# Kernel optimization log

Hardware: AMD Instinct MI355X
Metric: run time of the kernel (lower is better)

Reference implementation:

```python
import jax, jax.numpy as jnp
import numpy as np

N = 100000
E = 1600000
IN_C = 128
HID = 8
HEADS = 8
OUT_C = 40
NEG_SLOPE = 0.2


def _segment_softmax(e, seg, n):
    # e: [E, H], softmax over edges sharing the same destination `seg`
    m = jax.ops.segment_max(e, seg, num_segments=n)
    a = jnp.exp(e - m[seg])
    s = jax.ops.segment_sum(a, seg, num_segments=n)
    return a / (s[seg] + 1e-16)


def _gat_layer(x, src, dst, W, a_src, a_dst, b, heads, concat):
    # PyG GATConv (single-tensor input, shared lin for src/dst), self-loops pre-added.
    n = x.shape[0]
    c = W.shape[0] // heads
    h = (x @ W.T).reshape(n, heads, c)                     # [N, H, C]
    al_s = jnp.einsum('nhc,hc->nh', h, a_src)              # [N, H]
    al_d = jnp.einsum('nhc,hc->nh', h, a_dst)
    e = jax.nn.leaky_relu(al_s[src] + al_d[dst], NEG_SLOPE)  # [E, H]
    alpha = _segment_softmax(e, dst, n)                    # [E, H]
    out = jax.ops.segment_sum(alpha[:, :, None] * h[src], dst, num_segments=n)
    if concat:
        return out.reshape(n, heads * c) + b
    return out.mean(axis=1) + b


def setup_inputs() -> dict:
    key = jax.random.key(0)
    ks = jax.random.split(key, 24)
    HC = HEADS * HID
    def g(k, shape, fan_in):
        return jax.random.normal(k, shape, dtype=jnp.float32) * (1.0 / np.sqrt(fan_in))
    inp = {
        'x': jax.random.normal(ks[0], (N, IN_C), dtype=jnp.float32),
        'edge_index': jax.random.randint(ks[1], (2, E), 0, N, dtype=jnp.int32),
        # layer 0: in -> hidden x heads (concat)
        'W0': g(ks[2], (HC, IN_C), IN_C),
        'as0': g(ks[3], (HEADS, HID), HID),
        'ad0': g(ks[4], (HEADS, HID), HID),
        'b0': jnp.zeros((HC,), jnp.float32),
        'sW0': g(ks[5], (HC, IN_C), IN_C),
        'sb0': jnp.zeros((HC,), jnp.float32),
        # layer 1: HC -> hidden x heads (concat)
        'W1': g(ks[6], (HC, HC), HC),
        'as1': g(ks[7], (HEADS, HID), HID),
        'ad1': g(ks[8], (HEADS, HID), HID),
        'b1': jnp.zeros((HC,), jnp.float32),
        'sW1': g(ks[9], (HC, HC), HC),
        'sb1': jnp.zeros((HC,), jnp.float32),
        # layer 2: HC -> out (concat=False, mean over heads)
        'W2': g(ks[10], (HEADS * OUT_C, HC), HC),
        'as2': g(ks[11], (HEADS, OUT_C), OUT_C),
        'ad2': g(ks[12], (HEADS, OUT_C), OUT_C),
        'b2': jnp.zeros((OUT_C,), jnp.float32),
        'sW2': g(ks[13], (OUT_C, HC), HC),
        'sb2': jnp.zeros((OUT_C,), jnp.float32),
    }
    return inp


def reference(x, edge_index, W0, as0, ad0, b0, sW0, sb0,
              W1, as1, ad1, b1, sW1, sb1,
              W2, as2, ad2, b2, sW2, sb2):
    n = x.shape[0]
    loop = jnp.arange(n, dtype=edge_index.dtype)
    src = jnp.concatenate([edge_index[0], loop])  # add_self_loops=True (PyG default)
    dst = jnp.concatenate([edge_index[1], loop])

    # layer 0
    h = _gat_layer(x, src, dst, W0, as0, ad0, b0, HEADS, True) + (x @ sW0.T + sb0)
    h = jax.nn.elu(h)  # dropout is identity in eval mode
    # layer 1
    h = _gat_layer(h, src, dst, W1, as1, ad1, b1, HEADS, True) + (h @ sW1.T + sb1)
    h = jax.nn.elu(h)
    # layer 2 (concat=False)
    out = _gat_layer(h, src, dst, W2, as2, ad2, b2, HEADS, False) + (h @ sW2.T + sb2)
    return jax.nn.log_softmax(out, axis=-1)
```

## Files before the change

kernel.cpp:

```cpp
#include <hip/hip_runtime.h>
#include <hip/hip_bf16.h>
#include <math.h>

#define HEADS 8
#define NEG_SLOPE 0.2f

typedef __attribute__((ext_vector_type(8))) short short8v;
typedef __attribute__((ext_vector_type(4))) float f32x4;

__device__ __forceinline__ float bf2f(unsigned short u) {
    return __uint_as_float(((unsigned int)u) << 16);
}
__device__ __forceinline__ unsigned short f2bf(float f) {
    __hip_bfloat16 h = __float2bfloat16(f);
    union { __hip_bfloat16 h; unsigned short u; } c; c.h = h; return c.u;
}

__global__ void k_count(const int* __restrict__ ei, int* __restrict__ deg, int E) {
    int i = blockIdx.x * 256 + threadIdx.x;
    if (i < E) atomicAdd(&deg[ei[E + i]], 1);
}

__global__ void k_scan_block(const int* __restrict__ deg, int* __restrict__ offs,
                             int* __restrict__ bsum, int N) {
    __shared__ int lds[256];
    int tid = threadIdx.x;
    int base = blockIdx.x * 1024 + tid * 4;
    int v0 = (base + 0 < N) ? deg[base + 0] + 1 : 0;
    int v1 = (base + 1 < N) ? deg[base + 1] + 1 : 0;
    int v2 = (base + 2 < N) ? deg[base + 2] + 1 : 0;
    int v3 = (base + 3 < N) ? deg[base + 3] + 1 : 0;
    int t01 = v0 + v1;
    int tot = t01 + v2 + v3;
    lds[tid] = tot;
    __syncthreads();
    for (int off = 1; off < 256; off <<= 1) {
        int x = 0;
        if (tid >= off) x = lds[tid - off];
        __syncthreads();
        lds[tid] += x;
        __syncthreads();
    }
    int ex = lds[tid] - tot;
    if (tid == 255) bsum[blockIdx.x] = lds[255];
    if (base + 0 < N) offs[base + 0] = ex;
    if (base + 1 < N) offs[base + 1] = ex + v0;
    if (base + 2 < N) offs[base + 2] = ex + t01;
    if (base + 3 < N) offs[base + 3] = ex + t01 + v2;
}

__global__ void k_scan_top(int* __restrict__ bsum, int nb) {
    __shared__ int lds[256];
    int tid = threadIdx.x;
    int v = (tid < nb) ? bsum[tid] : 0;
    lds[tid] = v;
    __syncthreads();
    for (int off = 1; off < 256; off <<= 1) {
        int x = 0;
        if (tid >= off) x = lds[tid - off];
        __syncthreads();
        lds[tid] += x;
        __syncthreads();
    }
    if (tid < nb) bsum[tid] = lds[tid] - v;
    if (tid == 0) bsum[nb] = lds[255];
}

__global__ void k_scan_add(int* __restrict__ offs, int* __restrict__ cur,
                           const int* __restrict__ bsum, int N) {
    int i = blockIdx.x * 256 + threadIdx.x;
    if (i < N) {
        int v = offs[i] + bsum[i >> 10];
        offs[i] = v;
        cur[i] = v;
    }
    if (i == 0) offs[N] = bsum[(N + 1023) >> 10];
}

__global__ void k_scatter(const int* __restrict__ ei, int* __restrict__ cur,
                          int* __restrict__ csr, int E, int ET) {
    int i = blockIdx.x * 256 + threadIdx.x;
    if (i >= ET) return;
    int s, d;
    if (i < E) { s = ei[i]; d = ei[E + i]; }
    else       { s = d = i - E; }
    int pos = atomicAdd(&cur[d], 1);
    csr[pos] = s;
}

template <int CPT, int M1, int M2, bool AL_FOLD, bool A_BF16>
__global__ __launch_bounds__(256) void k_gemm_dual(
    const float* __restrict__ X, const float* __restrict__ Wa, const float* __restrict__ Wb,
    const float* __restrict__ bias1, const float* __restrict__ bias2,
    void* __restrict__ outa_, float* __restrict__ outb,
    const float* __restrict__ as_w, const float* __restrict__ ad_w, float* __restrict__ AL,
    int N, int K) {
    constexpr int M = M1 + M2;
    static_assert(CPT * 16 >= M, "CPT too small");
    __shared__ float sW[CPT * 16][68];
    __shared__ float sX[64][68];
    int tx = threadIdx.x, ty = threadIdx.y;
    int tid = ty * 16 + tx;
    int r0 = blockIdx.x * 64;

    float acc[4][CPT];
#pragma unroll
    for (int jc = 0; jc < CPT; ++jc) {
        int col = tx + 16 * jc;
        float b = 0.f;
        if (col >= M1 && col < M) b = bias1[col - M1] + bias2[col - M1];
#pragma unroll
        for (int jr = 0; jr < 4; ++jr) acc[jr][jc] = b;
    }

    for (int k0 = 0; k0 < K; k0 += 64) {
        __syncthreads();
        for (int idx = tid; idx < CPT * 16 * 16; idx += 256) {
            int c = idx >> 4, kq = (idx & 15) * 4;
            float4 v = make_float4(0.f, 0.f, 0.f, 0.f);
            if (c < M1) v = *(const float4*)&Wa[(size_t)c * K + k0 + kq];
            else if (c < M) v = *(const float4*)&Wb[(size_t)(c - M1) * K + k0 + kq];
            *(float4*)&sW[c][kq] = v;
        }
        for (int idx = tid; idx < 64 * 16; idx += 256) {
            int r = idx >> 4, kq = (idx & 15) * 4;
            int gr = r0 + r;
            float4 v = make_float4(0.f, 0.f, 0.f, 0.f);
            if (gr < N) v = *(const float4*)&X[(size_t)gr * K + k0 + kq];
            *(float4*)&sX[r][kq] = v;
        }
        __syncthreads();

        for (int k = 0; k < 64; k += 4) {
            float4 xr[4];
#pragma unroll
            for (int jr = 0; jr < 4; ++jr) xr[jr] = *(const float4*)&sX[ty * 4 + jr][k];
#pragma unroll
            for (int jc = 0; jc < CPT; ++jc) {
                float4 wc = *(const float4*)&sW[tx + 16 * jc][k];
#pragma unroll
                for (int jr = 0; jr < 4; ++jr)
                    acc[jr][jc] += wc.x * xr[jr].x + wc.y * xr[jr].y +
                                   wc.z * xr[jr].z + wc.w * xr[jr].w;
            }
        }
    }

#pragma unroll
    for (int jr = 0; jr < 4; ++jr) {
        int gr = r0 + ty * 4 + jr;
        if (gr >= N) continue;
#pragma unroll
        for (int jc = 0; jc < CPT; ++jc) {
            int col = tx + 16 * jc;
            if (col < M1) {
                if (A_BF16) ((unsigned short*)outa_)[(size_t)gr * M1 + col] = f2bf(acc[jr][jc]);
                else        ((float*)outa_)[(size_t)gr * M1 + col] = acc[jr][jc];
            } else if (col < M) {
                outb[(size_t)gr * M2 + (col - M1)] = acc[jr][jc];
            }
        }
    }

    if constexpr (AL_FOLD) {
        __syncthreads();
        float* sH = &sW[0][0];
#pragma unroll
        for (int jr = 0; jr < 4; ++jr)
#pragma unroll
            for (int jc = 0; jc < 4; ++jc)
                sH[(ty * 4 + jr) * 68 + (tx + 16 * jc)] = acc[jr][jc];
        __syncthreads();
        int j = tid & 15, hd = j & 7;
        const float* a = (j < 8 ? as_w : ad_w) + hd * 8;
        float av[8];
#pragma unroll
        for (int c = 0; c < 8; ++c) av[c] = a[c];
#pragma unroll
        for (int q = 0; q < 4; ++q) {
            int row = (tid >> 4) + 16 * q;
            int gr = r0 + row;
            if (gr < N) {
                float sum = 0.f;
#pragma unroll
                for (int c = 0; c < 8; ++c) sum += av[c] * sH[row * 68 + hd * 8 + c];
                AL[(size_t)gr * 16 + j] = sum;
            }
        }
    }
}

__global__ void k_prep2(const float* __restrict__ W2, const float* __restrict__ as2,
                        const float* __restrict__ ad2, float* __restrict__ wt,
                        __hip_bfloat16* __restrict__ w2sw) {
    if (blockIdx.x < 96) {
        int t = blockIdx.x * 256 + threadIdx.x;
        int j = t & 7;
        int rc = t >> 3;
        int col = rc % 48, c = rc / 48;
        int k = c * 8 + j;
        int hd = k >> 6, kk = k & 63;
        float v = (col < 40) ? W2[(size_t)(hd * 40 + col) * 64 + kk] : 0.f;
        w2sw[t] = __float2bfloat16(v);
    } else {
        for (int t = threadIdx.x; t < 1024; t += 256) {
            int j = t >> 6, k = t & 63;
            int hd = j & 7;
            const float* a = (j < 8 ? as2 : ad2) + hd * 40;
            float sum = 0.f;
            for (int c = 0; c < 40; ++c) sum += a[c] * W2[(size_t)(hd * 40 + c) * 64 + k];
            wt[j * 64 + k] = sum;
        }
    }
}

__global__ __launch_bounds__(256, 8) void k_fused(
    const unsigned short* __restrict__ Hb, const float* __restrict__ AL,
    const int* __restrict__ offs, const int* __restrict__ csr,
    float* __restrict__ S, unsigned short* __restrict__ Sb, int N) {
    int wid = threadIdx.x >> 6, lane = threadIdx.x & 63;
    int n = blockIdx.x * 4 + wid;
    if (n >= N) return;
    int off = offs[n], deg = offs[n + 1] - off;
    int el = lane >> 3, hd = lane & 7;
    int dp = lane & 31, es = lane >> 5;
    int hp = dp >> 2;
    float ald = AL[(size_t)n * 16 + 8 + hd];

    int src_c = 0; float e_c = 0.f;
    if (el < deg) {
        src_c = csr[off + el];
        float t = AL[(size_t)src_c * 16 + hd] + ald;
        e_c = __expf(t > 0.f ? t : NEG_SLOPE * t);
    }

    float s_run = 0.f, ax = 0.f, ay = 0.f;
    for (int b0 = 0; b0 < deg; b0 += 8) {
        unsigned int hv[4];
#pragma unroll
        for (int j = 0; j < 4; ++j) {
            int sj = __shfl(src_c, (2 * j + es) * 8);
            hv[j] = *(const unsigned int*)&Hb[(size_t)sj * 64 + 2 * dp];
        }
        int en = b0 + 8 + el;
        int src_n = 0; float e_n = 0.f;
        if (en < deg) {
            src_n = csr[off + en];
            float t = AL[(size_t)src_n * 16 + hd] + ald;
            e_n = __expf(t > 0.f ? t : NEG_SLOPE * t);
        }

        s_run += e_c;
#pragma unroll
        for (int j = 0; j < 4; ++j) {
            float a = __shfl(e_c, (2 * j + es) * 8 + hp);
            unsigned int u = hv[j];
            ax += a * bf2f((unsigned short)(u & 0xffff));
            ay += a * bf2f((unsigned short)(u >> 16));
        }
        src_c = src_n; e_c = e_n;
    }
#pragma unroll
    for (int d = 8; d <= 32; d <<= 1) s_run += __shfl_xor(s_run, d);
    float sf = __shfl(s_run, hp);
    float inv = 1.0f / (sf + 1e-16f);
    ax *= inv; ay *= inv;
    ax += __shfl_xor(ax, 32);
    ay += __shfl_xor(ay, 32);
    if (es == 0) {
        float2 sk = *(const float2*)&S[(size_t)n * 64 + 2 * dp];
        float vx = sk.x + ax, vy = sk.y + ay;
        vx = vx > 0.f ? vx : expm1f(vx);
        vy = vy > 0.f ? vy : expm1f(vy);
        *(float2*)&S[(size_t)n * 64 + 2 * dp] = make_float2(vx, vy);
        if (Sb) {
            ushort2 w;
            w.x = f2bf(vx); w.y = f2bf(vy);
            *(ushort2*)&Sb[(size_t)n * 64 + 2 * dp] = w;
        }
    }
}

__global__ __launch_bounds__(256, 8) void k_l2f(
    const unsigned short* __restrict__ Xb, const float* __restrict__ AL,
    const float* __restrict__ SK, const __hip_bfloat16* __restrict__ w2sw,
    const int* __restrict__ offs, const int* __restrict__ csr,
    float* __restrict__ out, int N) {
    __shared__ __hip_bfloat16 sA[64 * 16 * 8];
    __shared__ float sC[16][48];
    __shared__ float sW8[4][64];
    int wid = threadIdx.x >> 6, lane = threadIdx.x & 63;
    int el = lane >> 3, hd = lane & 7;
    int dp = lane & 31, eh = lane >> 5;

#pragma unroll 1
    for (int p = 0; p < 4; ++p) {
        int mrow = wid * 4 + p;
        int n = blockIdx.x * 16 + mrow;
        float2 acc[4];
#pragma unroll
        for (int h2 = 0; h2 < 4; ++h2) acc[h2] = make_float2(0.f, 0.f);
        if (n < N) {
            int off = offs[n], deg = offs[n + 1] - off;
            float ald = AL[(size_t)n * 16 + 8 + hd];

            int src_c = 0; float e_c = 0.f;
            if (el < deg) {
                src_c = csr[off + el];
                float t = AL[(size_t)src_c * 16 + hd] + ald;
                e_c = __expf(t > 0.f ? t : NEG_SLOPE * t);
            }

            float s_run = 0.f;
#pragma unroll 1
            for (int b0 = 0; b0 < deg; b0 += 8) {
                unsigned int xv0[4];
#pragma unroll
                for (int j = 0; j < 4; ++j) {
                    int sj = __shfl(src_c, j * 8);
                    xv0[j] = *(const unsigned int*)&Xb[(size_t)sj * 64 + 2 * dp];
                }
                int en = b0 + 8 + el;
                int src_n = 0; float e_n = 0.f;
                if (en < deg) {
                    src_n = csr[off + en];
                    float t = AL[(size_t)src_n * 16 + hd] + ald;
                    e_n = __expf(t > 0.f ? t : NEG_SLOPE * t);
                }

                sW8[wid][lane] = e_c;
                s_run += e_c;
#pragma unroll
                for (int j = 0; j < 4; ++j) {
                    float4 a4 = *(const float4*)&sW8[wid][j * 8 + 4 * eh];
                    float hx = bf2f((unsigned short)(xv0[j] & 0xffff));
                    float hy = bf2f((unsigned short)(xv0[j] >> 16));
                    acc[0].x += a4.x * hx; acc[0].y += a4.x * hy;
                    acc[1].x += a4.y * hx; acc[1].y += a4.y * hy;
                    acc[2].x += a4.z * hx; acc[2].y += a4.z * hy;
                    acc[3].x += a4.w * hx; acc[3].y += a4.w * hy;
                }
#pragma unroll
                for (int j = 0; j < 4; ++j) {
                    int sj = __shfl(src_c, (j + 4) * 8);
                    xv0[j] = *(const unsigned int*)&Xb[(size_t)sj * 64 + 2 * dp];
                }
#pragma unroll
                for (int j = 0; j < 4; ++j) {
                    float4 a4 = *(const float4*)&sW8[wid][(j + 4) * 8 + 4 * eh];
                    float hx = bf2f((unsigned short)(xv0[j] & 0xffff));
                    float hy = bf2f((unsigned short)(xv0[j] >> 16));
                    acc[0].x += a4.x * hx; acc[0].y += a4.x * hy;
                    acc[1].x += a4.y * hx; acc[1].y += a4.y * hy;
                    acc[2].x += a4.z * hx; acc[2].y += a4.z * hy;
                    acc[3].x += a4.w * hx; acc[3].y += a4.w * hy;
                }
                src_c = src_n; e_c = e_n;
            }
#pragma unroll
            for (int d = 8; d <= 32; d <<= 1) s_run += __shfl_xor(s_run, d);
#pragma unroll
            for (int h2 = 0; h2 < 4; ++h2) {
                float sv = __shfl(s_run, 4 * eh + h2);
                float iv = 1.0f / (sv + 1e-16f);
                acc[h2].x *= iv; acc[h2].y *= iv;
            }
        }
#pragma unroll
        for (int h2 = 0; h2 < 4; ++h2) {
            int K0 = (4 * eh + h2) * 64 + 2 * dp;
            int chunk = K0 >> 3, pos = K0 & 7;
            ushort2 w;
            w.x = f2bf(acc[h2].x); w.y = f2bf(acc[h2].y);
            *(ushort2*)&sA[chunk * 128 + ((mrow + chunk) & 15) * 8 + pos] = w;
        }
    }
    __syncthreads();

    if (wid < 3) {
        f32x4 cacc = {0.f, 0.f, 0.f, 0.f};
        int grp = lane >> 4;
        int r16 = lane & 15;
#pragma unroll 4
        for (int ks = 0; ks < 16; ++ks) {
            int c = ks * 4 + grp;
            short8v av = *(const short8v*)&sA[c * 128 + ((r16 + c) & 15) * 8];
            short8v bv = *(const short8v*)&w2sw[(size_t)(c * 48 + wid * 16 + r16) * 8];
            cacc = __builtin_amdgcn_mfma_f32_16x16x32_bf16(av, bv, cacc, 0, 0, 0);
        }
#pragma unroll
        for (int jj = 0; jj < 4; ++jj)
            sC[grp * 4 + jj][wid * 16 + r16] = cacc[jj];
    }
    __syncthreads();

    for (int p = 0; p < 4; ++p) {
        int mrow = wid * 4 + p;
        int n = blockIdx.x * 16 + mrow;
        if (n >= N) continue;
        float val = (lane < 40) ? SK[(size_t)n * 40 + lane] + sC[mrow][lane] * 0.125f : -INFINITY;
        float mx = val;
#pragma unroll
        for (int d = 32; d; d >>= 1) mx = fmaxf(mx, __shfl_xor(mx, d));
        float ex = (lane < 40) ? __expf(val - mx) : 0.f;
        float sm = ex;
#pragma unroll
        for (int d = 32; d; d >>= 1) sm += __shfl_xor(sm, d);
        if (lane < 40) out[(size_t)n * 40 + lane] = val - mx - logf(sm);
    }
}

extern "C" void kernel_launch(void* const* d_in, const int* in_sizes, int n_in,
                              void* d_out, int out_size, void* d_ws, size_t ws_size,
                              hipStream_t stream) {
    const float* x   = (const float*)d_in[0];
    const int*   ei  = (const int*)d_in[1];
    const float* W0  = (const float*)d_in[2];
    const float* as0 = (const float*)d_in[3];
    const float* ad0 = (const float*)d_in[4];
    const float* b0  = (const float*)d_in[5];
    const float* sW0 = (const float*)d_in[6];
    const float* sb0 = (const float*)d_in[7];
    const float* W1  = (const float*)d_in[8];
    const float* as1 = (const float*)d_in[9];
    const float* ad1 = (const float*)d_in[10];
    const float* b1  = (const float*)d_in[11];
    const float* sW1 = (const float*)d_in[12];
    const float* sb1 = (const float*)d_in[13];
    const float* W2  = (const float*)d_in[14];
    const float* as2 = (const float*)d_in[15];
    const float* ad2 = (const float*)d_in[16];
    const float* b2  = (const float*)d_in[17];
    const float* sW2 = (const float*)d_in[18];
    const float* sb2 = (const float*)d_in[19];
    float* out = (float*)d_out;

    int N = in_sizes[0] / 128;
    int E = in_sizes[1] / 2;
    int ET = E + N;

    char* wsp = (char*)d_ws;
    size_t woff = 0;
    auto A = [&](size_t nbytes) -> void* {
        void* p = wsp + woff;
        woff = (woff + nbytes + 255) & ~(size_t)255;
        return p;
    };
    int* offs   = (int*)A((size_t)(N + 1) * 4);
    int* cur    = (int*)A((size_t)N * 4);
    int* deg    = (int*)A((size_t)N * 4);
    int* bsum   = (int*)A(4096);
    int* csr    = (int*)A((size_t)ET * 4);
    float* wt   = (float*)A(1024 * 4);
    __hip_bfloat16* w2sw = (__hip_bfloat16*)A(64 * 48 * 8 * 2);
    float* AL   = (float*)A((size_t)N * 16 * 4);
    float* S    = (float*)A((size_t)N * 64 * 4);
    float* T    = (float*)A((size_t)N * 64 * 4);
    unsigned short* Hb = (unsigned short*)A((size_t)N * 64 * 2);
    unsigned short* Tb = (unsigned short*)A((size_t)N * 64 * 2);
    (void)ws_size; (void)n_in; (void)out_size;

    hipMemsetAsync(deg, 0, (size_t)N * 4, stream);
    k_count<<<(E + 255) / 256, 256, 0, stream>>>(ei, deg, E);
    int nb = (N + 1023) / 1024;
    k_scan_block<<<nb, 256, 0, stream>>>(deg, offs, bsum, N);
    k_scan_top<<<1, 256, 0, stream>>>(bsum, nb);
    k_scan_add<<<(N + 255) / 256, 256, 0, stream>>>(offs, cur, bsum, N);
    k_scatter<<<(ET + 255) / 256, 256, 0, stream>>>(ei, cur, csr, E, ET);

    k_prep2<<<97, 256, 0, stream>>>(W2, as2, ad2, wt, w2sw);

    dim3 bG(16, 16);
    int gG = (N + 63) / 64;
    int gN4 = (N + 3) / 4;

    k_gemm_dual<8, 64, 64, true, true><<<gG, bG, 0, stream>>>(
        x, W0, sW0, b0, sb0, Hb, S, as0, ad0, AL, N, 128);
    k_fused<<<gN4, 256, 0, stream>>>(Hb, AL, offs, csr, S, nullptr, N);

    k_gemm_dual<8, 64, 64, true, true><<<gG, bG, 0, stream>>>(
        S, W1, sW1, b1, sb1, Hb, T, as1, ad1, AL, N, 64);
    k_fused<<<gN4, 256, 0, stream>>>(Hb, AL, offs, csr, T, Tb, N);

    k_gemm_dual<4, 16, 40, false, false><<<gG, bG, 0, stream>>>(
        T, wt, sW2, b2, sb2, AL, S, nullptr, nullptr, nullptr, N, 64);
    k_l2f<<<(N + 15) / 16, 256, 0, stream>>>(Tb, AL, S, w2sw, offs, csr, out, N);
}
```

Before: 568.6 us.

## Build CSR via two-pass destination binning with LDS-local rank assignment

Replaces the global-atomic scatter pass with a two-stage build. First, edges are binned into fixed-size slack buckets of 64 destinations each, while degrees are counted in the same pass. Second, one block per bucket assigns ranks with shared-memory atomics and writes self-loops first. This cuts random global atomics and scattered writes into the CSR. The cost is an extra record buffer, and edges are silently dropped if a bucket overflows SLACK entries.

New measurement: 690.8 us. +21.5%, slower.

```diff
diff --git a/kernel.cpp b/kernel.cpp
--- a/kernel.cpp
+++ b/kernel.cpp
@@ -4,6 +4,8 @@
 
 #define HEADS 8
 #define NEG_SLOPE 0.2f
+#define BSHIFT 6
+#define SLACK 2048
 
 typedef __attribute__((ext_vector_type(8))) short short8v;
 typedef __attribute__((ext_vector_type(4))) float f32x4;
@@ -16,9 +18,15 @@
     union { __hip_bfloat16 h; unsigned short u; } c; c.h = h; return c.u;
 }
 
-__global__ void k_count(const int* __restrict__ ei, int* __restrict__ deg, int E) {
+__global__ void k_binA(const int* __restrict__ ei, int* __restrict__ deg,
+                       int* __restrict__ bcnt, int2* __restrict__ rec, int E) {
     int i = blockIdx.x * 256 + threadIdx.x;
-    if (i < E) atomicAdd(&deg[ei[E + i]], 1);
+    if (i >= E) return;
+    int s = ei[i], d = ei[E + i];
+    atomicAdd(&deg[d], 1);
+    int b = d >> BSHIFT;
+    int pos = atomicAdd(&bcnt[b], 1);
+    if (pos < SLACK) rec[(size_t)b * SLACK + pos] = make_int2(s, d);
 }
 
 __global__ void k_scan_block(const int* __restrict__ deg, int* __restrict__ offs,
@@ -66,26 +74,38 @@
     if (tid == 0) bsum[nb] = lds[255];
 }
 
-__global__ void k_scan_add(int* __restrict__ offs, int* __restrict__ cur,
-                           const int* __restrict__ bsum, int N) {
+__global__ void k_scan_add(int* __restrict__ offs, const int* __restrict__ bsum, int N) {
     int i = blockIdx.x * 256 + threadIdx.x;
-    if (i < N) {
-        int v = offs[i] + bsum[i >> 10];
-        offs[i] = v;
-        cur[i] = v;
-    }
+    if (i < N) offs[i] += bsum[i >> 10];
     if (i == 0) offs[N] = bsum[(N + 1023) >> 10];
 }
 
-__global__ void k_scatter(const int* __restrict__ ei, int* __restrict__ cur,
-                          int* __restrict__ csr, int E, int ET) {
-    int i = blockIdx.x * 256 + threadIdx.x;
-    if (i >= ET) return;
-    int s, d;
-    if (i < E) { s = ei[i]; d = ei[E + i]; }
-    else       { s = d = i - E; }
-    int pos = atomicAdd(&cur[d], 1);
-    csr[pos] = s;
+__global__ __launch_bounds__(256) void k_binB(
+    const int2* __restrict__ rec, const int* __restrict__ bcnt,
+    const int* __restrict__ offs, int* __restrict__ csr, int N) {
+    __shared__ int loff[64];
+    __shared__ int lcnt[64];
+    int b = blockIdx.x;
+    int tid = threadIdx.x;
+    int n0 = b << BSHIFT;
+    if (tid < 64) {
+        lcnt[tid] = 0;
+        int n = n0 + tid;
+        if (n < N) {
+            int o = offs[n];
+            loff[tid] = o;
+            csr[o] = n;
+        }
+    }
+    __syncthreads();
+    int cnt = min(bcnt[b], SLACK);
+    const int2* base = rec + (size_t)b * SLACK;
+    for (int i = tid; i < cnt; i += 256) {
+        int2 r = base[i];
+        int l = r.y & 63;
+        int rank = atomicAdd(&lcnt[l], 1);
+        csr[loff[l] + 1 + rank] = r.x;
+    }
 }
 
 template <int CPT, int M1, int M2, bool AL_FOLD, bool A_BF16>
@@ -437,7 +457,7 @@
 
     int N = in_sizes[0] / 128;
     int E = in_sizes[1] / 2;
-    int ET = E + N;
+    int NB = (N + 63) >> BSHIFT;
 
     char* wsp = (char*)d_ws;
     size_t woff = 0;
@@ -447,10 +467,11 @@
         return p;
     };
     int* offs   = (int*)A((size_t)(N + 1) * 4);
-    int* cur    = (int*)A((size_t)N * 4);
     int* deg    = (int*)A((size_t)N * 4);
     int* bsum   = (int*)A(4096);
-    int* csr    = (int*)A((size_t)ET * 4);
+    int* bcnt   = (int*)A((size_t)(NB + 1) * 4);
+    int* csr    = (int*)A((size_t)(E + N) * 4);
+    int2* rec   = (int2*)A((size_t)NB * SLACK * 8);
     float* wt   = (float*)A(1024 * 4);
     __hip_bfloat16* w2sw = (__hip_bfloat16*)A(64 * 48 * 8 * 2);
     float* AL   = (float*)A((size_t)N * 16 * 4);
@@ -461,12 +482,13 @@
     (void)ws_size; (void)n_in; (void)out_size;
 
     hipMemsetAsync(deg, 0, (size_t)N * 4, stream);
-    k_count<<<(E + 255) / 256, 256, 0, stream>>>(ei, deg, E);
+    hipMemsetAsync(bcnt, 0, (size_t)(NB + 1) * 4, stream);
+    k_binA<<<(E + 255) / 256, 256, 0, stream>>>(ei, deg, bcnt, rec, E);
     int nb = (N + 1023) / 1024;
     k_scan_block<<<nb, 256, 0, stream>>>(deg, offs, bsum, N);
     k_scan_top<<<1, 256, 0, stream>>>(bsum, nb);
-    k_scan_add<<<(N + 255) / 256, 256, 0, stream>>>(offs, cur, bsum, N);
-    k_scatter<<<(ET + 255) / 256, 256, 0, stream>>>(ei, cur, csr, E, ET);
+    k_scan_add<<<(N + 255) / 256, 256, 0, stream>>>(offs, bsum, N);
+    k_binB<<<NB, 256, 0, stream>>>(rec, bcnt, offs, csr, N);
 
     k_prep2<<<97, 256, 0, stream>>>(W2, as2, ad2, wt, w2sw);
 
```
